# Optimization experiments

Hardware: AMD Instinct MI355X
Metric: run time of the kernel (lower is better)

Reference implementation:

```python
import jax, jax.numpy as jnp
import numpy as np

N_NODES = 50000
N_EDGES = 800000
NUM_FEATURES = 128
DIM_HIDDEN = 128
DIM_OUT = 64


def setup_inputs() -> dict:
    key = jax.random.key(0)
    k = jax.random.split(key, 5)
    x = jax.random.normal(k[0], (N_NODES, NUM_FEATURES), dtype=jnp.float32)
    edge_index = jax.random.randint(k[1], (2, N_EDGES), 0, N_NODES, dtype=jnp.int32)
    W1 = jax.random.normal(k[2], (NUM_FEATURES, DIM_HIDDEN), dtype=jnp.float32) * (1.0 / np.sqrt(NUM_FEATURES))
    b1 = jnp.zeros((DIM_HIDDEN,), dtype=jnp.float32)
    W2 = jax.random.normal(k[3], (DIM_HIDDEN, DIM_OUT), dtype=jnp.float32) * (1.0 / np.sqrt(DIM_HIDDEN))
    b2 = jnp.zeros((DIM_OUT,), dtype=jnp.float32)
    return {"x": x, "edge_index": edge_index, "W1": W1, "b1": b1, "W2": W2, "b2": b2}


def _gcn_conv(x, W, b, src, dst, n_nodes):
    # PyG GCNConv: out = D^{-1/2} (A+I) D^{-1/2} X W + b (self-loops already in src/dst)
    deg = jax.ops.segment_sum(jnp.ones_like(dst, dtype=x.dtype), dst, num_segments=n_nodes)
    dinv = jax.lax.rsqrt(jnp.maximum(deg, 1.0))  # deg >= 1 thanks to self-loops
    norm = dinv[src] * dinv[dst]                 # [E]
    xw = x @ W                                   # dense GEMM on nodes [N, out]
    msg = xw[src] * norm[:, None]                # gather + edge-wise scale [E, out]
    out = jax.ops.segment_sum(msg, dst, num_segments=n_nodes)  # scatter-add
    return out + b


def reference(x, edge_index, W1, b1, W2, b2):
    n = x.shape[0]
    loops = jnp.arange(n, dtype=edge_index.dtype)
    src = jnp.concatenate([edge_index[0], loops])
    dst = jnp.concatenate([edge_index[1], loops])
    h = _gcn_conv(x, W1, b1, src, dst, n)
    h = jax.nn.relu(h)
    h = _gcn_conv(h, W2, b2, src, dst, n)
    return jax.nn.log_softmax(h, axis=1)
```

## Files before the change

kernel.cpp:

```cpp
#include <hip/hip_runtime.h>
#include <cstdint>
#include <cstddef>


#define N_FEAT 128
#define NWAVE 8192

__device__ __forceinline__ unsigned f2bf(float f) {
  unsigned u = __float_as_uint(f);
  return (u + 0x7FFFu + ((u >> 16) & 1u)) >> 16;
}
__device__ __forceinline__ float bflo(unsigned u) { return __uint_as_float(u << 16); }
__device__ __forceinline__ float bfhi(unsigned u) { return __uint_as_float(u & 0xFFFF0000u); }

__global__ void k_hist(const int* __restrict__ dst, int* __restrict__ cnt,
                       int* __restrict__ rank, int E) {
  int e = blockIdx.x * blockDim.x + threadIdx.x;
  if (e < E) rank[e] = atomicAdd(&cnt[dst[e]], 1);
}

__global__ __launch_bounds__(256) void k_bsum(const int* __restrict__ cnt,
                                              int* __restrict__ bsum, int n) {
  int i = blockIdx.x * 256 + threadIdx.x;
  int v = (i < n) ? ((cnt[i] + 3) & ~3) : 0;
  for (int o = 32; o > 0; o >>= 1) v += __shfl_down(v, o);
  __shared__ int w[4];
  if ((threadIdx.x & 63) == 0) w[threadIdx.x >> 6] = v;
  __syncthreads();
  if (threadIdx.x == 0) bsum[blockIdx.x] = w[0] + w[1] + w[2] + w[3];
}

__global__ __launch_bounds__(256) void k_bscan(const int* __restrict__ bsum,
                                               int* __restrict__ bbase, int nb) {
  __shared__ int lds[256];
  int t = threadIdx.x;
  int v = (t < nb) ? bsum[t] : 0;
  lds[t] = v;
  __syncthreads();
  for (int o = 1; o < 256; o <<= 1) {
    int u = (t >= o) ? lds[t - o] : 0;
    __syncthreads();
    lds[t] += u;
    __syncthreads();
  }
  if (t < nb) bbase[t] = lds[t] - v;
}

__global__ __launch_bounds__(256) void k_scan2(const int* __restrict__ cnt,
                                               const int* __restrict__ bbase,
                                               int* __restrict__ rowptr,
                                               float* __restrict__ dinv,
                                               unsigned* __restrict__ desc, int n) {
  __shared__ int lds[256];
  int t = threadIdx.x;
  int i = blockIdx.x * 256 + t;
  int c  = (i < n) ? cnt[i] : 0;
  int pc = (c + 3) & ~3;
  lds[t] = pc;
  __syncthreads();
  for (int o = 1; o < 256; o <<= 1) {
    int u = (t >= o) ? lds[t - o] : 0;
    __syncthreads();
    lds[t] += u;
    __syncthreads();
  }
  if (i < n) {
    int excl = bbase[blockIdx.x] + lds[t] - pc;
    rowptr[i] = excl;
    dinv[i] = rsqrtf((float)(c + 1));
    for (int p = excl + c; p < excl + pc; ++p) desc[p] = 0;
    if (i == n - 1) rowptr[n] = excl + pc;
  }
}

__global__ void k_wstart(const int* __restrict__ rowptr, int* __restrict__ wstart, int n) {
  int w = blockIdx.x * blockDim.x + threadIdx.x;
  if (w > NWAVE) return;
  if (w == NWAVE) { wstart[w] = n; return; }
  long long target = (long long)rowptr[n] * w / NWAVE;
  int lo = 0, hi = n;
  while (lo < hi) {
    int mid = (lo + hi) >> 1;
    if (rowptr[mid] < (int)target) lo = mid + 1; else hi = mid;
  }
  wstart[w] = lo;
}

__global__ void k_fill(const int* __restrict__ src, const int* __restrict__ dst,
                       const int* __restrict__ rank, const int* __restrict__ rowptr,
                       const float* __restrict__ dinv,
                       unsigned* __restrict__ desc, int E) {
  int e = blockIdx.x * blockDim.x + threadIdx.x;
  if (e >= E) return;
  int s = src[e], d = dst[e];
  int p = rowptr[d] + rank[e];
  desc[p] = (f2bf(dinv[s] * dinv[d]) << 16) | (unsigned)s;
}

__global__ __launch_bounds__(256) void k_gemm1(const float* __restrict__ X,
                                               const float* __restrict__ W,
                                               unsigned short* __restrict__ Yb, int n) {
  __shared__ float XlT[128][20];
  int row0 = blockIdx.x * 16;
  for (int it = 0; it < 8; ++it) {
    int idx = threadIdx.x + it * 256;
    int r = idx >> 7, k = idx & 127;
    int row = row0 + r;
    XlT[k][r] = (row < n) ? X[(size_t)row * 128 + k] : 0.0f;
  }
  __syncthreads();
  int j  = threadIdx.x & 127;
  int rs = (threadIdx.x >> 7) * 8;
  float acc[8];
#pragma unroll
  for (int a = 0; a < 8; ++a) acc[a] = 0.0f;
#pragma unroll 4
  for (int k = 0; k < 128; ++k) {
    float w = W[k * 128 + j];
    float4 a0 = *(const float4*)&XlT[k][rs];
    float4 a1 = *(const float4*)&XlT[k][rs + 4];
    acc[0] += a0.x * w; acc[1] += a0.y * w; acc[2] += a0.z * w; acc[3] += a0.w * w;
    acc[4] += a1.x * w; acc[5] += a1.y * w; acc[6] += a1.z * w; acc[7] += a1.w * w;
  }
#pragma unroll
  for (int a = 0; a < 8; ++a) {
    int row = row0 + rs + a;
    if (row < n) Yb[(size_t)row * 128 + j] = (unsigned short)f2bf(acc[a]);
  }
}

__global__ __launch_bounds__(256) void k_gemm2(const unsigned* __restrict__ Hu,
                                               const float* __restrict__ W,
                                               unsigned short* __restrict__ Yb, int n) {
  __shared__ float XlT[128][20];
  int row0 = blockIdx.x * 16;
  for (int it = 0; it < 4; ++it) {
    int idx = threadIdx.x + it * 256;
    int r = idx >> 6, k2 = idx & 63;
    int row = row0 + r;
    unsigned u = (row < n) ? Hu[(size_t)row * 64 + k2] : 0u;
    XlT[2 * k2][r]     = bflo(u);
    XlT[2 * k2 + 1][r] = bfhi(u);
  }
  __syncthreads();
  int j  = threadIdx.x & 63;
  int rs = (threadIdx.x >> 6) * 4;
  float acc[4];
#pragma unroll
  for (int a = 0; a < 4; ++a) acc[a] = 0.0f;
#pragma unroll 4
  for (int k = 0; k < 128; ++k) {
    float w = W[k * 64 + j];
    float4 a0 = *(const float4*)&XlT[k][rs];
    acc[0] += a0.x * w; acc[1] += a0.y * w; acc[2] += a0.z * w; acc[3] += a0.w * w;
  }
#pragma unroll
  for (int a = 0; a < 4; ++a) {
    int row = row0 + rs + a;
    if (row < n) Yb[(size_t)row * 64 + j] = (unsigned short)f2bf(acc[a]);
  }
}

__global__ __launch_bounds__(256) void k_agg128(const unsigned* __restrict__ desc,
                                                const int* __restrict__ rowptr,
                                                const int* __restrict__ wstart,
                                                const float* __restrict__ dinv,
                                                const float* __restrict__ bias,
                                                const unsigned* __restrict__ xwb,
                                                unsigned* __restrict__ hb, int n) {
  int w    = (blockIdx.x * blockDim.x + threadIdx.x) >> 6;
  int lane = threadIdx.x & 63;
  if (w >= NWAVE) return;
  int r0 = wstart[w], r1 = wstart[w + 1];
  if (r0 >= r1) return;
  float bx0 = bias[2 * lane], bx1 = bias[2 * lane + 1];
  int beg = rowptr[r0];
  for (int r = r0; r < r1; ++r) {
    int end = rowptr[r + 1];
    float di = dinv[r];
    float sl = di * di;
    unsigned us = xwb[(size_t)r * 64 + lane];
    float ax = bx0 + bflo(us) * sl;
    float ay = bx1 + bfhi(us) * sl;
    float bx = 0.0f, by = 0.0f;
    for (int base = beg; base < end; base += 4) {
      uint4 d4 = *(const uint4*)(desc + base);
      unsigned u0 = xwb[(size_t)(d4.x & 0xFFFFu) * 64 + lane];
      unsigned u1 = xwb[(size_t)(d4.y & 0xFFFFu) * 64 + lane];
      unsigned u2 = xwb[(size_t)(d4.z & 0xFFFFu) * 64 + lane];
      unsigned u3 = xwb[(size_t)(d4.w & 0xFFFFu) * 64 + lane];
      float n0 = bfhi(d4.x), n1 = bfhi(d4.y), n2 = bfhi(d4.z), n3 = bfhi(d4.w);
      ax += bflo(u0) * n0; ay += bfhi(u0) * n0;
      bx += bflo(u1) * n1; by += bfhi(u1) * n1;
      ax += bflo(u2) * n2; ay += bfhi(u2) * n2;
      bx += bflo(u3) * n3; by += bfhi(u3) * n3;
    }
    float ox = fmaxf(ax + bx, 0.0f), oy = fmaxf(ay + by, 0.0f);
    hb[(size_t)r * 64 + lane] = f2bf(ox) | (f2bf(oy) << 16);
    beg = end;
  }
}

__global__ __launch_bounds__(256) void k_agg64ls(const unsigned* __restrict__ desc,
                                                 const int* __restrict__ rowptr,
                                                 const int* __restrict__ wstart,
                                                 const float* __restrict__ dinv,
                                                 const float* __restrict__ bias,
                                                 const unsigned* __restrict__ hwb,
                                                 float* __restrict__ out, int n) {
  int w    = (blockIdx.x * blockDim.x + threadIdx.x) >> 6;
  int lane = threadIdx.x & 63;
  if (w >= NWAVE) return;
  int r0 = wstart[w], r1 = wstart[w + 1];
  if (r0 >= r1) return;
  int c    = lane & 31;
  int half = lane >> 5;
  float bc0 = bias[2 * c], bc1 = bias[2 * c + 1];
  int beg = rowptr[r0];
  for (int r = r0; r < r1; ++r) {
    int end = rowptr[r + 1];
    float ax = 0.0f, ay = 0.0f, bx = 0.0f, by = 0.0f;
    if (half == 0) {
      float di = dinv[r];
      unsigned us = hwb[(size_t)r * 32 + c];
      ax = bc0 + bflo(us) * di * di;
      ay = bc1 + bfhi(us) * di * di;
    }
    for (int base = beg; base < end; base += 4) {
      uint4 d4 = *(const uint4*)(desc + base);
      unsigned dA = half ? d4.z : d4.x;
      unsigned dB = half ? d4.w : d4.y;
      unsigned uA = hwb[(size_t)(dA & 0xFFFFu) * 32 + c];
      unsigned uB = hwb[(size_t)(dB & 0xFFFFu) * 32 + c];
      float nA = bfhi(dA), nB = bfhi(dB);
      ax += bflo(uA) * nA; ay += bfhi(uA) * nA;
      bx += bflo(uB) * nB; by += bfhi(uB) * nB;
    }
    float vx = ax + bx, vy = ay + by;
    vx += __shfl_xor(vx, 32);
    vy += __shfl_xor(vy, 32);
    float m = fmaxf(vx, vy);
    for (int o = 16; o > 0; o >>= 1) m = fmaxf(m, __shfl_xor(m, o));
    float s = expf(vx - m) + expf(vy - m);
    for (int o = 16; o > 0; o >>= 1) s += __shfl_xor(s, o);
    float ls = logf(s);
    if (half == 0) {
      float2 o2 = { vx - m - ls, vy - m - ls };
      *(float2*)(out + (size_t)r * 64 + 2 * c) = o2;
    }
    beg = end;
  }
}

extern "C" void kernel_launch(void* const* d_in, const int* in_sizes, int n_in,
                              void* d_out, int out_size, void* d_ws, size_t ws_size,
                              hipStream_t stream) {
  const float* x  = (const float*)d_in[0];
  const int*   ei = (const int*)d_in[1];
  const float* W1 = (const float*)d_in[2];
  const float* b1 = (const float*)d_in[3];
  const float* W2 = (const float*)d_in[4];
  const float* b2 = (const float*)d_in[5];
  float* out = (float*)d_out;

  const int n = in_sizes[0] / N_FEAT;
  const int E = in_sizes[1] / 2;
  const int* src = ei;
  const int* dst = ei + E;
  const int nb = (n + 255) / 256;

  auto align = [](size_t v) { return (v + 255) & ~(size_t)255; };
  char* ws = (char*)d_ws;
  size_t off = 0;
  int*      cnt    = (int*)     (ws + off); off += align((size_t)n * 4);
  int*      rowptr = (int*)     (ws + off); off += align((size_t)(n + 1) * 4);
  float*    dinv   = (float*)   (ws + off); off += align((size_t)n * 4);
  int*      rank   = (int*)     (ws + off); off += align((size_t)E * 4);
  int*      bsum   = (int*)     (ws + off); off += align(256 * 4);
  int*      bbase  = (int*)     (ws + off); off += align(256 * 4);
  int*      wstart = (int*)     (ws + off); off += align((size_t)(NWAVE + 1) * 4);
  unsigned* desc   = (unsigned*)(ws + off); off += align((size_t)(E + 4 * n) * 4);
  unsigned* xwb    = (unsigned*)(ws + off); off += align((size_t)n * 64 * 4);
  unsigned* hb     = (unsigned*)(ws + off); off += align((size_t)n * 64 * 4);
  unsigned* hwb    = xwb;

  hipMemsetAsync(cnt, 0, (size_t)n * 4, stream);
  k_hist<<<(E + 255) / 256, 256, 0, stream>>>(dst, cnt, rank, E);
  k_bsum<<<nb, 256, 0, stream>>>(cnt, bsum, n);
  k_bscan<<<1, 256, 0, stream>>>(bsum, bbase, nb);
  k_scan2<<<nb, 256, 0, stream>>>(cnt, bbase, rowptr, dinv, desc, n);
  k_wstart<<<(NWAVE + 256) / 256, 256, 0, stream>>>(rowptr, wstart, n);
  k_fill<<<(E + 255) / 256, 256, 0, stream>>>(src, dst, rank, rowptr, dinv, desc, E);

  k_gemm1<<<(n + 15) / 16, 256, 0, stream>>>(x, W1, (unsigned short*)xwb, n);
  k_agg128<<<NWAVE / 4, 256, 0, stream>>>(desc, rowptr, wstart, dinv, b1, xwb, hb, n);

  k_gemm2<<<(n + 15) / 16, 256, 0, stream>>>(hb, W2, (unsigned short*)hwb, n);
  k_agg64ls<<<NWAVE / 4, 256, 0, stream>>>(desc, rowptr, wstart, dinv, b2, hwb, out, n);
}
```

Baseline: 260.0 us.

## Replace scalar FP32 GEMMs with templated bf16 MFMA kernel

Both dense node GEMMs move from scalar FP32 FMA loops to one templated kernel built on the 16x16x32 bf16 MFMA instruction. X and W tiles are converted to bf16 and staged in LDS with an XOR swizzle to avoid bank conflicts, and 64 rows are processed per block. The aim is to cut the compute cost of the GEMM stages, at the price of rounding the FP32 input x and the weights to bf16 before the multiply.

Measured after the change: 231.2 us. -11.1%, faster.

```diff
diff --git a/kernel.cpp b/kernel.cpp
--- a/kernel.cpp
+++ b/kernel.cpp
@@ -6,12 +6,16 @@
 #define N_FEAT 128
 #define NWAVE 8192
 
+typedef short bf16x8 __attribute__((ext_vector_type(8)));
+typedef float f32x4 __attribute__((ext_vector_type(4)));
+
 __device__ __forceinline__ unsigned f2bf(float f) {
   unsigned u = __float_as_uint(f);
   return (u + 0x7FFFu + ((u >> 16) & 1u)) >> 16;
 }
 __device__ __forceinline__ float bflo(unsigned u) { return __uint_as_float(u << 16); }
 __device__ __forceinline__ float bfhi(unsigned u) { return __uint_as_float(u & 0xFFFF0000u); }
+
 
 __global__ void k_hist(const int* __restrict__ dst, int* __restrict__ cnt,
                        int* __restrict__ rank, int E) {
@@ -97,69 +101,76 @@
   desc[p] = (f2bf(dinv[s] * dinv[d]) << 16) | (unsigned)s;
 }
 
-__global__ __launch_bounds__(256) void k_gemm1(const float* __restrict__ X,
-                                               const float* __restrict__ W,
-                                               unsigned short* __restrict__ Yb, int n) {
-  __shared__ float XlT[128][20];
-  int row0 = blockIdx.x * 16;
-  for (int it = 0; it < 8; ++it) {
-    int idx = threadIdx.x + it * 256;
-    int r = idx >> 7, k = idx & 127;
-    int row = row0 + r;
-    XlT[k][r] = (row < n) ? X[(size_t)row * 128 + k] : 0.0f;
+template<int NCOL, bool XF32>
+__global__ __launch_bounds__(256) void k_gemm_mfma(const void* __restrict__ Xv,
+                                                   const float* __restrict__ W,
+                                                   unsigned short* __restrict__ Yb,
+                                                   int n) {
+  constexpr int NT = NCOL / 16;
+  __shared__ uint4 Xl[64][16];
+  __shared__ uint4 Wl[NCOL][16];
+  int t = threadIdx.x;
+  int row0 = blockIdx.x * 64;
+
+  for (int c = t; c < 1024; c += 256) {
+    int lr = c >> 4, kc = c & 15;
+    int row = row0 + lr;
+    uint4 v = {0u, 0u, 0u, 0u};
+    if (row < n) {
+      if constexpr (XF32) {
+        const float* Xf = (const float*)Xv;
+        float4 f0 = *(const float4*)(Xf + (size_t)row * 128 + kc * 8);
+        float4 f1 = *(const float4*)(Xf + (size_t)row * 128 + kc * 8 + 4);
+        v.x = f2bf(f0.x) | (f2bf(f0.y) << 16);
+        v.y = f2bf(f0.z) | (f2bf(f0.w) << 16);
+        v.z = f2bf(f1.x) | (f2bf(f1.y) << 16);
+        v.w = f2bf(f1.z) | (f2bf(f1.w) << 16);
+      } else {
+        v = ((const uint4*)Xv)[(size_t)row * 16 + kc];
+      }
+    }
+    Xl[lr][kc ^ (lr & 7)] = v;
+  }
+  {
+    int j = t % NCOL, kc0 = t / NCOL;
+    for (int kc = kc0; kc < 16; kc += 256 / NCOL) {
+      const float* wp = W + (size_t)(kc * 8) * NCOL + j;
+      float f[8];
+#pragma unroll
+      for (int e = 0; e < 8; ++e) f[e] = wp[e * NCOL];
+      uint4 v;
+      v.x = f2bf(f[0]) | (f2bf(f[1]) << 16);
+      v.y = f2bf(f[2]) | (f2bf(f[3]) << 16);
+      v.z = f2bf(f[4]) | (f2bf(f[5]) << 16);
+      v.w = f2bf(f[6]) | (f2bf(f[7]) << 16);
+      Wl[j][kc ^ (j & 7)] = v;
+    }
   }
   __syncthreads();
-  int j  = threadIdx.x & 127;
-  int rs = (threadIdx.x >> 7) * 8;
-  float acc[8];
-#pragma unroll
-  for (int a = 0; a < 8; ++a) acc[a] = 0.0f;
-#pragma unroll 4
-  for (int k = 0; k < 128; ++k) {
-    float w = W[k * 128 + j];
-    float4 a0 = *(const float4*)&XlT[k][rs];
-    float4 a1 = *(const float4*)&XlT[k][rs + 4];
-    acc[0] += a0.x * w; acc[1] += a0.y * w; acc[2] += a0.z * w; acc[3] += a0.w * w;
-    acc[4] += a1.x * w; acc[5] += a1.y * w; acc[6] += a1.z * w; acc[7] += a1.w * w;
-  }
-#pragma unroll
-  for (int a = 0; a < 8; ++a) {
-    int row = row0 + rs + a;
-    if (row < n) Yb[(size_t)row * 128 + j] = (unsigned short)f2bf(acc[a]);
-  }
-}
-
-__global__ __launch_bounds__(256) void k_gemm2(const unsigned* __restrict__ Hu,
-                                               const float* __restrict__ W,
-                                               unsigned short* __restrict__ Yb, int n) {
-  __shared__ float XlT[128][20];
-  int row0 = blockIdx.x * 16;
-  for (int it = 0; it < 4; ++it) {
-    int idx = threadIdx.x + it * 256;
-    int r = idx >> 6, k2 = idx & 63;
-    int row = row0 + r;
-    unsigned u = (row < n) ? Hu[(size_t)row * 64 + k2] : 0u;
-    XlT[2 * k2][r]     = bflo(u);
-    XlT[2 * k2 + 1][r] = bfhi(u);
-  }
-  __syncthreads();
-  int j  = threadIdx.x & 63;
-  int rs = (threadIdx.x >> 6) * 4;
-  float acc[4];
-#pragma unroll
-  for (int a = 0; a < 4; ++a) acc[a] = 0.0f;
-#pragma unroll 4
-  for (int k = 0; k < 128; ++k) {
-    float w = W[k * 64 + j];
-    float4 a0 = *(const float4*)&XlT[k][rs];
-    acc[0] += a0.x * w; acc[1] += a0.y * w; acc[2] += a0.z * w; acc[3] += a0.w * w;
-  }
-#pragma unroll
-  for (int a = 0; a < 4; ++a) {
-    int row = row0 + rs + a;
-    if (row < n) Yb[(size_t)row * 64 + j] = (unsigned short)f2bf(acc[a]);
-  }
-}
+
+  int w = t >> 6, lane = t & 63;
+  int lr16 = lane & 15, kg = lane >> 4;
+  bf16x8 a[4];
+#pragma unroll
+  for (int kk = 0; kk < 4; ++kk)
+    a[kk] = __builtin_bit_cast(bf16x8, Xl[w * 16 + lr16][(kk * 4 + kg) ^ (lane & 7)]);
+#pragma unroll
+  for (int jt = 0; jt < NT; ++jt) {
+    f32x4 acc = {0.0f, 0.0f, 0.0f, 0.0f};
+#pragma unroll
+    for (int kk = 0; kk < 4; ++kk) {
+      bf16x8 b = __builtin_bit_cast(bf16x8, Wl[jt * 16 + lr16][(kk * 4 + kg) ^ (lane & 7)]);
+      acc = __builtin_amdgcn_mfma_f32_16x16x32_bf16(a[kk], b, acc, 0, 0, 0);
+    }
+    int col = jt * 16 + lr16;
+#pragma unroll
+    for (int r = 0; r < 4; ++r) {
+      int row = row0 + w * 16 + kg * 4 + r;
+      if (row < n) Yb[(size_t)row * NCOL + col] = (unsigned short)f2bf(acc[r]);
+    }
+  }
+}
+
 
 __global__ __launch_bounds__(256) void k_agg128(const unsigned* __restrict__ desc,
                                                 const int* __restrict__ rowptr,
@@ -292,9 +303,11 @@
   k_wstart<<<(NWAVE + 256) / 256, 256, 0, stream>>>(rowptr, wstart, n);
   k_fill<<<(E + 255) / 256, 256, 0, stream>>>(src, dst, rank, rowptr, dinv, desc, E);
 
-  k_gemm1<<<(n + 15) / 16, 256, 0, stream>>>(x, W1, (unsigned short*)xwb, n);
+  k_gemm_mfma<128, true><<<(n + 63) / 64, 256, 0, stream>>>(
+      x, W1, (unsigned short*)xwb, n);
   k_agg128<<<NWAVE / 4, 256, 0, stream>>>(desc, rowptr, wstart, dinv, b1, xwb, hb, n);
 
-  k_gemm2<<<(n + 15) / 16, 256, 0, stream>>>(hb, W2, (unsigned short*)hwb, n);
+  k_gemm_mfma<64, false><<<(n + 63) / 64, 256, 0, stream>>>(
+      hb, W2, (unsigned short*)hwb, n);
   k_agg64ls<<<NWAVE / 4, 256, 0, stream>>>(desc, rowptr, wstart, dinv, b2, hwb, out, n);
 }
```
